# Kernel optimization log

Hardware: AMD Instinct MI355X
Metric: run time of the kernel (lower is better)

## Reference

```python
import jax, jax.numpy as jnp
import numpy as np

NUM_HEADS = 16
NUM_KV_HEADS = 4
HEAD_DIM = 128
HIDDEN = 2048
SEQ = 2048
BATCH = 2
Q_PER_GROUP = NUM_HEADS // NUM_KV_HEADS          # 4
GROUP_SIZE = (Q_PER_GROUP + 2) * HEAD_DIM        # 768
TOTAL_PROJ = NUM_KV_HEADS * GROUP_SIZE           # 3072


def setup_inputs() -> dict:
    key = jax.random.key(0)
    k1, k2, k3 = jax.random.split(key, 3)
    x = jax.random.normal(k1, (SEQ, BATCH, HIDDEN), dtype=jnp.float32)
    w_qkv = jax.random.normal(k2, (TOTAL_PROJ, HIDDEN), dtype=jnp.float32) * 0.02
    w_proj = jax.random.normal(k3, (HIDDEN, NUM_HEADS * HEAD_DIM), dtype=jnp.float32) * 0.02
    return {"x": x, "w_qkv": w_qkv, "w_proj": w_proj}


def reference(x, w_qkv, w_proj):
    s, b, _ = x.shape
    # fused QKV projection (GQA-packed layout: per kv-group [q...q, k, v])
    qkv = jnp.einsum('sbh,ph->sbp', x, w_qkv)                       # [s,b,3072]
    qkv = qkv.reshape(s, b, NUM_KV_HEADS, GROUP_SIZE)
    q = qkv[..., :Q_PER_GROUP * HEAD_DIM].reshape(s, b, NUM_HEADS, HEAD_DIM)
    k = qkv[..., Q_PER_GROUP * HEAD_DIM:(Q_PER_GROUP + 1) * HEAD_DIM]  # [s,b,kvh,d]
    v = qkv[..., (Q_PER_GROUP + 1) * HEAD_DIM:]                        # [s,b,kvh,d]
    # to [b, heads, s, d]; expand kv heads over query groups (GQA)
    q = q.transpose(1, 2, 0, 3)
    k = jnp.repeat(k.transpose(1, 2, 0, 3), Q_PER_GROUP, axis=1)
    v = jnp.repeat(v.transpose(1, 2, 0, 3), Q_PER_GROUP, axis=1)
    scale = 1.0 / jnp.sqrt(jnp.asarray(HEAD_DIM, dtype=x.dtype))
    scores = jnp.einsum('bhsd,bhtd->bhst', q, k) * scale           # [b,h,s,s]
    attn = jax.nn.softmax(scores, axis=-1)
    out = jnp.einsum('bhst,bhtd->bhsd', attn, v)                    # [b,h,s,d]
    out = out.transpose(2, 0, 1, 3).reshape(s, b, NUM_HEADS * HEAD_DIM)
    return jnp.einsum('sbe,he->sbh', out, w_proj)                   # [s,b,hidden]
```

## Files before the change

### kernel.cpp

```cpp
#include <hip/hip_runtime.h>
#include <hip/hip_bf16.h>

typedef __bf16 bf16;
typedef __bf16 bf16x8 __attribute__((ext_vector_type(8)));
typedef __bf16 bf16x4v __attribute__((ext_vector_type(4)));
typedef float  f32x4  __attribute__((ext_vector_type(4)));
typedef float  f32x16 __attribute__((ext_vector_type(16)));

#define SEQL  2048
#define BATCH 2
#define HID   2048
#define NH    16
#define NKVH  4
#define HD    128
#define NPROJ 3072
#define MROWS 4096

#define QSCALE (0.08838834764831845f * 1.44269504088896340f)

__device__ __forceinline__ void gload16(const void* src, void* dst) {
  __builtin_amdgcn_global_load_lds(
      (__attribute__((address_space(1))) void*)src,
      (__attribute__((address_space(3))) void*)dst, 16, 0, 0);
}

__device__ __forceinline__ int swz128(int off) { return off ^ (((off >> 7) & 7) << 4); }
__device__ __forceinline__ int swz256(int off) { return off ^ (((off >> 8) & 7) << 4); }

__device__ __forceinline__ unsigned cvtpk_bf16(float lo, float hi) {
  unsigned r;
  asm("v_cvt_pk_bf16_f32 %0, %1, %2" : "=v"(r) : "v"(lo), "v"(hi));
  return r;
}
__device__ __forceinline__ void permswap32(unsigned& a, unsigned& b) {
  asm volatile("v_permlane32_swap_b32 %0, %1" : "+v"(a), "+v"(b));
}
__device__ __forceinline__ f32x16 mfma16(bf16x8 a, bf16x8 b, f32x16 c) {
  return __builtin_amdgcn_mfma_f32_32x32x16_bf16(a, b, c, 0, 0, 0);
}

__global__ __launch_bounds__(256) void cvt_kernel(
    const float* __restrict__ x, const float* __restrict__ wq, const float* __restrict__ wp,
    bf16* __restrict__ xo, bf16* __restrict__ wqo, bf16* __restrict__ wpo) {
  const int NXQ  = (MROWS * HID) / 4;
  const int NWQQ = (NPROJ * HID) / 4;
  const int NWPQ = (HID * HID) / 4;
  const int total = NXQ + NWQQ + NWPQ;
  for (int i = blockIdx.x * blockDim.x + threadIdx.x; i < total; i += gridDim.x * blockDim.x) {
    const float4* src; bf16* dst; int j;
    if (i < NXQ)            { src = (const float4*)x;  dst = xo;  j = i; }
    else if (i < NXQ + NWQQ){ src = (const float4*)wq; dst = wqo; j = i - NXQ; }
    else                    { src = (const float4*)wp; dst = wpo; j = i - NXQ - NWQQ; }
    float4 v = src[j];
    bf16x4v o;
    o[0] = (bf16)v.x; o[1] = (bf16)v.y; o[2] = (bf16)v.z; o[3] = (bf16)v.w;
    *(bf16x4v*)(dst + (size_t)j * 4) = o;
  }
}

__global__ __launch_bounds__(256, 3) void qkv_gemm(
    const bf16* __restrict__ A, const bf16* __restrict__ B,
    bf16* __restrict__ Qo, bf16* __restrict__ Ko, bf16* __restrict__ Vt) {
  __shared__ char lds[32768];
  const int tid = threadIdx.x, l = tid & 63, w = tid >> 6;
  const int lin = blockIdx.x + 24 * blockIdx.y;
  const int swz = (lin & 7) * 96 + (lin >> 3);
  const int bx = swz % 24, by = swz / 24;
  const int r0 = by * 128, p0 = bx * 128;
  const int wr = w >> 1, wc = w & 1;

  f32x4 acc[4][4];
  const f32x4 fzero = {0.f, 0.f, 0.f, 0.f};
#pragma unroll
  for (int m = 0; m < 4; m++)
#pragma unroll
    for (int n = 0; n < 4; n++) acc[m][n] = fzero;

  for (int kt = 0; kt < HID / 64; ++kt) {
    const int k0 = kt * 64;
    __syncthreads();
#pragma unroll
    for (int q = 0; q < 4; q++) {
      const int doff = (w * 4 + q) * 1024 + l * 16;
      const int row = doff >> 7;
      const int chv = ((doff >> 4) & 7) ^ (row & 7);
      gload16((const char*)A + ((size_t)(r0 + row) * HID + k0) * 2 + chv * 16,
              lds + (w * 4 + q) * 1024);
      gload16((const char*)B + ((size_t)(p0 + row) * HID + k0) * 2 + chv * 16,
              lds + 16384 + (w * 4 + q) * 1024);
    }
    __syncthreads();
    bf16x8 af[4][2], bfr[4][2];
#pragma unroll
    for (int m = 0; m < 4; m++)
#pragma unroll
      for (int kk = 0; kk < 2; kk++) {
        int off = (wr * 64 + m * 16 + (l & 15)) * 128 + kk * 64 + (l >> 4) * 16;
        af[m][kk] = *(const bf16x8*)(lds + swz128(off));
      }
#pragma unroll
    for (int n = 0; n < 4; n++)
#pragma unroll
      for (int kk = 0; kk < 2; kk++) {
        int off = (wc * 64 + n * 16 + (l & 15)) * 128 + kk * 64 + (l >> 4) * 16;
        bfr[n][kk] = *(const bf16x8*)(lds + 16384 + swz128(off));
      }
#pragma unroll
    for (int kk = 0; kk < 2; kk++)
#pragma unroll
      for (int m = 0; m < 4; m++)
#pragma unroll
        for (int n = 0; n < 4; n++)
          acc[m][n] = __builtin_amdgcn_mfma_f32_16x16x32_bf16(af[m][kk], bfr[n][kk], acc[m][n], 0, 0, 0);
  }

  const int seg = (p0 % 768) / 128;
  const int g = p0 / 768;
#pragma unroll
  for (int m = 0; m < 4; m++) {
    const int rbase = r0 + wr * 64 + m * 16 + ((l >> 4) << 2);
#pragma unroll
    for (int n = 0; n < 4; n++) {
      const int c = wc * 64 + n * 16 + (l & 15);
#pragma unroll
      for (int rg = 0; rg < 4; ++rg) {
        const int r = rbase + rg;
        const int s = r >> 1, b = r & 1;
        if (seg < 4) {
          const int h = g * 4 + seg;
          Qo[(((size_t)(b * 16 + h)) * 2048 + s) * 128 + c] = (bf16)(acc[m][n][rg] * QSCALE);
        } else if (seg == 4) {
          Ko[(((size_t)(b * 4 + g)) * 2048 + s) * 128 + c] = (bf16)acc[m][n][rg];
        } else {
          Vt[(((size_t)(b * 4 + g)) * 128 + c) * 2048 + s] = (bf16)acc[m][n][rg];
        }
      }
    }
  }
}

template<int BASE>
__device__ __forceinline__ void attn_tile(
    char* lds, const bf16x8* qf, const int* ka, const int* va,
    f32x16* oacc, f32x16& lacc, bf16x8 ones) {
  const f32x16 z16 = {};

  f32x16 sT0 = z16, sT1 = z16;
  __builtin_amdgcn_s_setprio(1);
#pragma unroll
  for (int s = 0; s < 8; s++) {
    bf16x8 kf = *(const bf16x8*)(lds + BASE + ka[s]);
    sT0 = mfma16(kf, qf[s], sT0);
  }
#pragma unroll
  for (int s = 0; s < 8; s++) {
    bf16x8 kf = *(const bf16x8*)(lds + BASE + ka[8 + s]);
    sT1 = mfma16(kf, qf[s], sT1);
  }
  __builtin_amdgcn_s_setprio(0);

#pragma unroll
  for (int i = 0; i < 16; i++) sT0[i] = exp2f(sT0[i]);
#pragma unroll
  for (int i = 0; i < 16; i++) sT1[i] = exp2f(sT1[i]);

  unsigned c0[8], c1[8];
#pragma unroll
  for (int i = 0; i < 8; i++) c0[i] = cvtpk_bf16(sT0[2 * i], sT0[2 * i + 1]);
#pragma unroll
  for (int i = 0; i < 8; i++) c1[i] = cvtpk_bf16(sT1[2 * i], sT1[2 * i + 1]);
  permswap32(c0[0], c0[2]); permswap32(c0[1], c0[3]);
  permswap32(c0[4], c0[6]); permswap32(c0[5], c0[7]);
  permswap32(c1[0], c1[2]); permswap32(c1[1], c1[3]);
  permswap32(c1[4], c1[6]); permswap32(c1[5], c1[7]);

  __builtin_amdgcn_s_setprio(1);
#pragma unroll
  for (int ks = 0; ks < 4; ks++) {
    union { unsigned u[4]; bf16x8 v; } pb;
    const unsigned* cs = (ks < 2) ? c0 : c1;
#pragma unroll
    for (int i = 0; i < 4; i++) pb.u[i] = cs[(ks & 1) * 4 + i];
    lacc = mfma16(ones, pb.v, lacc);
#pragma unroll
    for (int dblk = 0; dblk < 4; dblk++) {
      bf16x8 vf = *(const bf16x8*)(lds + BASE + 16384 + va[ks * 4 + dblk]);
      oacc[dblk] = mfma16(vf, pb.v, oacc[dblk]);
    }
  }
  __builtin_amdgcn_s_setprio(0);
}

__global__ __launch_bounds__(256, 2) void attn_kernel(
    const bf16* __restrict__ Q, const bf16* __restrict__ K, const bf16* __restrict__ V,
    bf16* __restrict__ O) {
  __shared__ char lds[65536];
  const int tid = threadIdx.x, l = tid & 63, w = tid >> 6;
  const int l31 = l & 31, h2 = l >> 5;
  const int lin = blockIdx.x + (blockIdx.y << 4);
  const int swzb = (lin & 7) * 64 + (lin >> 3);
  const int qt = swzb & 15, bh = swzb >> 4;
  const int b = bh >> 4, head = bh & 15, g = head >> 2;

  const int q0 = qt * 128 + w * 32;

  bf16x8 qf[8];
  {
    const bf16* qbase = Q + (((size_t)(b * 16 + head)) * 2048 + q0 + l31) * 128 + h2 * 8;
#pragma unroll
    for (int s = 0; s < 8; s++) qf[s] = *(const bf16x8*)(qbase + s * 16);
  }

  int ka[16], va[16];
#pragma unroll
  for (int tsub = 0; tsub < 2; tsub++)
#pragma unroll
    for (int s = 0; s < 8; s++)
      ka[tsub * 8 + s] = swz256((tsub * 32 + l31) * 256 + s * 32 + h2 * 16);
#pragma unroll
  for (int ks = 0; ks < 4; ks++)
#pragma unroll
    for (int dblk = 0; dblk < 4; dblk++)
      va[ks * 4 + dblk] = swz128((dblk * 32 + l31) * 128 + ks * 32 + h2 * 16);

  int kso[4], vso[4];
#pragma unroll
  for (int q = 0; q < 4; q++) {
    const int off = (q * 4 + w) * 1024 + l * 16;
    kso[q] = swz256(off);
    const int rowv = off >> 7;
    const int chv = ((off >> 4) & 7) ^ (rowv & 7);
    vso[q] = rowv * 4096 + chv * 16;
  }

  bf16x8 ones;
#pragma unroll
  for (int i = 0; i < 8; i++) ones[i] = (bf16)1.0f;

  const f32x16 z16 = {};
  f32x16 oacc[4];
#pragma unroll
  for (int d = 0; d < 4; d++) oacc[d] = z16;
  f32x16 lacc = z16;

  const char* kbase = (const char*)(K + ((size_t)(b * 4 + g)) * 2048 * 128);
  const char* vbase = (const char*)(V + ((size_t)(b * 4 + g)) * 128 * 2048);

  auto stage = [&](int t0, int B) {
#pragma unroll
    for (int q = 0; q < 4; q++) {
      gload16(kbase + (size_t)t0 * 256 + kso[q], lds + B + (q * 4 + w) * 1024);
      gload16(vbase + (size_t)t0 * 2 + vso[q], lds + B + 16384 + (q * 4 + w) * 1024);
    }
  };

  stage(0, 0);
  __syncthreads();

  for (int t0 = 0; t0 < SEQL; t0 += 128) {
    stage(t0 + 64, 32768);
    attn_tile<0>(lds, qf, ka, va, oacc, lacc, ones);
    __syncthreads();
    if (t0 + 128 < SEQL) stage(t0 + 128, 0);
    attn_tile<32768>(lds, qf, ka, va, oacc, lacc, ones);
    __syncthreads();
  }

  const float inv = 1.0f / lacc[0];
  const size_t rowo = ((size_t)(q0 + l31) * 2 + b) * 2048 + (size_t)head * 128;
#pragma unroll
  for (int dblk = 0; dblk < 4; dblk++)
#pragma unroll
    for (int g4 = 0; g4 < 4; g4++) {
      bf16x4v ov;
#pragma unroll
      for (int e = 0; e < 4; e++) ov[e] = (bf16)(oacc[dblk][g4 * 4 + e] * inv);
      *(bf16x4v*)(O + rowo + dblk * 32 + g4 * 8 + h2 * 4) = ov;
    }
}

__global__ __launch_bounds__(256, 2) void proj_gemm(
    const bf16* __restrict__ A, const bf16* __restrict__ B, float* __restrict__ C) {
  __shared__ char lds[32768];
  const int tid = threadIdx.x, l = tid & 63, w = tid >> 6;
  const int lin = blockIdx.x + (blockIdx.y << 4);
  const int swz = (lin & 7) * 64 + (lin >> 3);
  const int bx = swz & 15, by = swz >> 4;
  const int r0 = by * 128, p0 = bx * 128;
  const int wr = w >> 1, wc = w & 1;

  f32x4 acc[4][4];
  const f32x4 fzero = {0.f, 0.f, 0.f, 0.f};
#pragma unroll
  for (int m = 0; m < 4; m++)
#pragma unroll
    for (int n = 0; n < 4; n++) acc[m][n] = fzero;

  for (int kt = 0; kt < HID / 64; ++kt) {
    const int k0 = kt * 64;
    __syncthreads();
#pragma unroll
    for (int q = 0; q < 4; q++) {
      const int doff = (w * 4 + q) * 1024 + l * 16;
      const int row = doff >> 7;
      const int chv = ((doff >> 4) & 7) ^ (row & 7);
      gload16((const char*)A + ((size_t)(r0 + row) * HID + k0) * 2 + chv * 16,
              lds + (w * 4 + q) * 1024);
      gload16((const char*)B + ((size_t)(p0 + row) * HID + k0) * 2 + chv * 16,
              lds + 16384 + (w * 4 + q) * 1024);
    }
    __syncthreads();
    bf16x8 af[4][2], bfr[4][2];
#pragma unroll
    for (int m = 0; m < 4; m++)
#pragma unroll
      for (int kk = 0; kk < 2; kk++) {
        int off = (wr * 64 + m * 16 + (l & 15)) * 128 + kk * 64 + (l >> 4) * 16;
        af[m][kk] = *(const bf16x8*)(lds + swz128(off));
      }
#pragma unroll
    for (int n = 0; n < 4; n++)
#pragma unroll
      for (int kk = 0; kk < 2; kk++) {
        int off = (wc * 64 + n * 16 + (l & 15)) * 128 + kk * 64 + (l >> 4) * 16;
        bfr[n][kk] = *(const bf16x8*)(lds + 16384 + swz128(off));
      }
#pragma unroll
    for (int kk = 0; kk < 2; kk++)
#pragma unroll
      for (int m = 0; m < 4; m++)
#pragma unroll
        for (int n = 0; n < 4; n++)
          acc[m][n] = __builtin_amdgcn_mfma_f32_16x16x32_bf16(af[m][kk], bfr[n][kk], acc[m][n], 0, 0, 0);
  }
#pragma unroll
  for (int m = 0; m < 4; m++) {
    const int rbase = r0 + wr * 64 + m * 16 + ((l >> 4) << 2);
#pragma unroll
    for (int n = 0; n < 4; n++) {
      const int c = p0 + wc * 64 + n * 16 + (l & 15);
#pragma unroll
      for (int rg = 0; rg < 4; ++rg)
        C[(size_t)(rbase + rg) * HID + c] = acc[m][n][rg];
    }
  }
}

extern "C" void kernel_launch(void* const* d_in, const int* in_sizes, int n_in,
                              void* d_out, int out_size, void* d_ws, size_t ws_size,
                              hipStream_t stream) {
  const float* x  = (const float*)d_in[0];
  const float* wq = (const float*)d_in[1];
  const float* wp = (const float*)d_in[2];
  float* out = (float*)d_out;
  char* ws = (char*)d_ws;

  size_t off = 0;
  bf16* xb  = (bf16*)(ws + off); off += (size_t)MROWS * HID * 2;
  bf16* wqb = (bf16*)(ws + off); off += (size_t)NPROJ * HID * 2;
  bf16* wpb = (bf16*)(ws + off); off += (size_t)HID * HID * 2;
  bf16* Qb  = (bf16*)(ws + off); off += (size_t)2 * 16 * 2048 * 128 * 2;
  bf16* Kb  = (bf16*)(ws + off); off += (size_t)2 * 4 * 2048 * 128 * 2;
  bf16* Vb  = (bf16*)(ws + off); off += (size_t)2 * 4 * 128 * 2048 * 2;
  bf16* Ob  = xb;

  cvt_kernel<<<2048, 256, 0, stream>>>(x, wq, wp, xb, wqb, wpb);
  qkv_gemm<<<dim3(24, 32), 256, 0, stream>>>(xb, wqb, Qb, Kb, Vb);
  attn_kernel<<<dim3(16, 32), 256, 0, stream>>>(Qb, Kb, Vb, Ob);
  proj_gemm<<<dim3(16, 32), 256, 0, stream>>>(Ob, wpb, out);
}
```

Before: 205.6 us.

## Read V fragments directly from global memory instead of staging through LDS

```diff
diff --git a/kernel.cpp b/kernel.cpp
--- a/kernel.cpp
+++ b/kernel.cpp
@@ -141,7 +141,7 @@
 
 template<int BASE>
 __device__ __forceinline__ void attn_tile(
-    char* lds, const bf16x8* qf, const int* ka, const int* va,
+    char* lds, const bf16x8* qf, const int* ka, const char* vb, int t0,
     f32x16* oacc, f32x16& lacc, bf16x8 ones) {
   const f32x16 z16 = {};
 
@@ -174,6 +174,7 @@
   permswap32(c1[0], c1[2]); permswap32(c1[1], c1[3]);
   permswap32(c1[4], c1[6]); permswap32(c1[5], c1[7]);
 
+  const char* vt = vb + (size_t)t0 * 2;
   __builtin_amdgcn_s_setprio(1);
 #pragma unroll
   for (int ks = 0; ks < 4; ks++) {
@@ -184,7 +185,7 @@
     lacc = mfma16(ones, pb.v, lacc);
 #pragma unroll
     for (int dblk = 0; dblk < 4; dblk++) {
-      bf16x8 vf = *(const bf16x8*)(lds + BASE + 16384 + va[ks * 4 + dblk]);
+      bf16x8 vf = *(const bf16x8*)(vt + dblk * 131072 + ks * 32);
       oacc[dblk] = mfma16(vf, pb.v, oacc[dblk]);
     }
   }
@@ -194,7 +195,7 @@
 __global__ __launch_bounds__(256, 2) void attn_kernel(
     const bf16* __restrict__ Q, const bf16* __restrict__ K, const bf16* __restrict__ V,
     bf16* __restrict__ O) {
-  __shared__ char lds[65536];
+  __shared__ char lds[32768];
   const int tid = threadIdx.x, l = tid & 63, w = tid >> 6;
   const int l31 = l & 31, h2 = l >> 5;
   const int lin = blockIdx.x + (blockIdx.y << 4);
@@ -211,27 +212,16 @@
     for (int s = 0; s < 8; s++) qf[s] = *(const bf16x8*)(qbase + s * 16);
   }
 
-  int ka[16], va[16];
+  int ka[16];
 #pragma unroll
   for (int tsub = 0; tsub < 2; tsub++)
 #pragma unroll
     for (int s = 0; s < 8; s++)
       ka[tsub * 8 + s] = swz256((tsub * 32 + l31) * 256 + s * 32 + h2 * 16);
-#pragma unroll
-  for (int ks = 0; ks < 4; ks++)
-#pragma unroll
-    for (int dblk = 0; dblk < 4; dblk++)
-      va[ks * 4 + dblk] = swz128((dblk * 32 + l31) * 128 + ks * 32 + h2 * 16);
-
-  int kso[4], vso[4];
-#pragma unroll
-  for (int q = 0; q < 4; q++) {
-    const int off = (q * 4 + w) * 1024 + l * 16;
-    kso[q] = swz256(off);
-    const int rowv = off >> 7;
-    const int chv = ((off >> 4) & 7) ^ (rowv & 7);
-    vso[q] = rowv * 4096 + chv * 16;
-  }
+
+  int kso[4];
+#pragma unroll
+  for (int q = 0; q < 4; q++) kso[q] = swz256((q * 4 + w) * 1024 + l * 16);
 
   bf16x8 ones;
 #pragma unroll
@@ -244,25 +234,23 @@
   f32x16 lacc = z16;
 
   const char* kbase = (const char*)(K + ((size_t)(b * 4 + g)) * 2048 * 128);
-  const char* vbase = (const char*)(V + ((size_t)(b * 4 + g)) * 128 * 2048);
-
-  auto stage = [&](int t0, int B) {
-#pragma unroll
-    for (int q = 0; q < 4; q++) {
+  const char* vb = (const char*)(V + ((size_t)(b * 4 + g) * 128 + l31) * 2048) + h2 * 16;
+
+  auto stageK = [&](int t0, int B) {
+#pragma unroll
+    for (int q = 0; q < 4; q++)
       gload16(kbase + (size_t)t0 * 256 + kso[q], lds + B + (q * 4 + w) * 1024);
-      gload16(vbase + (size_t)t0 * 2 + vso[q], lds + B + 16384 + (q * 4 + w) * 1024);
-    }
   };
 
-  stage(0, 0);
+  stageK(0, 0);
   __syncthreads();
 
   for (int t0 = 0; t0 < SEQL; t0 += 128) {
-    stage(t0 + 64, 32768);
-    attn_tile<0>(lds, qf, ka, va, oacc, lacc, ones);
-    __syncthreads();
-    if (t0 + 128 < SEQL) stage(t0 + 128, 0);
-    attn_tile<32768>(lds, qf, ka, va, oacc, lacc, ones);
+    stageK(t0 + 64, 16384);
+    attn_tile<0>(lds, qf, ka, vb, t0, oacc, lacc, ones);
+    __syncthreads();
+    if (t0 + 128 < SEQL) stageK(t0 + 128, 0);
+    attn_tile<16384>(lds, qf, ka, vb, t0 + 64, oacc, lacc, ones);
     __syncthreads();
   }
 
```

After: 255.1 us. 1.24x slower.
